# Optimization experiments

Measured on AMD Instinct MI355X. Metric: run time of the kernel, lower is better.

The kernel has to match this reference:

```python
import jax, jax.numpy as jnp
import numpy as np

def setup_inputs() -> dict:
    key = jax.random.key(0)
    k1, k2, k3, k4 = jax.random.split(key, 4)
    B, T, C, D = 4, 4096, 1024, 128
    x = jax.random.normal(k1, (B, T, C), dtype=jnp.float32)
    Wq = jax.random.normal(k2, (C, D), dtype=jnp.float32) * (C ** -0.5)
    Wk = jax.random.normal(k3, (C, D), dtype=jnp.float32) * (C ** -0.5)
    Wv = jax.random.normal(k4, (C, D), dtype=jnp.float32) * (C ** -0.5)
    return {"x": x, "Wq": Wq, "Wk": Wk, "Wv": Wv}

def reference(x, Wq, Wk, Wv):
    # x: [B,T,C]; Wq/Wk/Wv: [C,D] (nn.Linear bias=False => x @ W)
    B, T, C = x.shape
    q = jnp.einsum('btc,cd->btd', x, Wq)  # [B,T,D]
    k = jnp.einsum('btc,cd->btd', x, Wk)
    v = jnp.einsum('btc,cd->btd', x, Wv)
    dk = q.shape[-1]
    scale = dk ** -0.5
    w = jnp.einsum('btd,bsd->bts', q, k) * scale  # [B,T,T]
    causal = jnp.tril(jnp.ones((T, T), dtype=bool))
    w = jnp.where(causal, w, -jnp.inf)
    w = jax.nn.softmax(w, axis=-1)
    # dropout p=0.0 => identity
    attention = jnp.einsum('bts,bsd->btd', w, v)  # [B,T,D]
    return attention
```

## Files before the change

### kernel.cpp

```cpp
#include <hip/hip_runtime.h>
#include <stdint.h>

typedef __bf16 bf16_t;
typedef bf16_t bf16x8 __attribute__((ext_vector_type(8)));
typedef float f32x4 __attribute__((ext_vector_type(4)));
typedef unsigned short us8 __attribute__((ext_vector_type(8)));
typedef unsigned short us4 __attribute__((ext_vector_type(4)));
typedef unsigned int u32x4 __attribute__((ext_vector_type(4)));

#define B_ 4
#define T_ 4096
#define C_ 1024
#define D_ 128

#define NCHUNK_PB 144
#define QSCALE 0.12751744f
#define M0 14.0f

__device__ __forceinline__ uint16_t f2bf(float f) {
    union { float f; uint32_t u; } v; v.f = f;
    uint32_t u = v.u;
    uint32_t r = (u + 0x7fffu + ((u >> 16) & 1u)) >> 16;
    return (uint16_t)r;
}

__device__ __forceinline__ uint16_t bfru(float f) {
    return (uint16_t)((__float_as_uint(f) + 0x8000u) >> 16);
}

__device__ __forceinline__ float bf2f(uint16_t u) {
    return __uint_as_float((uint32_t)u << 16);
}

__device__ __forceinline__ void gload_lds16(const void* g, void* l) {
    __builtin_amdgcn_global_load_lds(
        (const __attribute__((address_space(1))) void*)g,
        (__attribute__((address_space(3))) void*)l, 16, 0, 0);
}

__global__ __launch_bounds__(256) void prep_w(const float* __restrict__ Wq,
                                              const float* __restrict__ Wk,
                                              const float* __restrict__ Wv,
                                              uint16_t* __restrict__ WT) {
    int idx = blockIdx.x * 256 + threadIdx.x;
    if (idx >= 3 * D_ * C_) return;
    int w   = idx / (D_ * C_);
    int rem = idx - w * (D_ * C_);
    int n   = rem / C_;
    int k   = rem - n * C_;
    const float* W = (w == 0) ? Wq : (w == 1) ? Wk : Wv;
    WT[idx] = f2bf(W[(size_t)k * D_ + n]);
}

#define GST 72

__global__ __launch_bounds__(256) void qkv_gemm(const float* __restrict__ x,
                                                const uint16_t* __restrict__ WT,
                                                uint16_t* __restrict__ qb,
                                                uint16_t* __restrict__ kb,
                                                uint16_t* __restrict__ vT) {
    __shared__ __align__(16) uint16_t A_lds[64 * GST];
    __shared__ __align__(16) uint16_t W_lds[128 * GST];

    int tid  = threadIdx.x;
    int lane = tid & 63;
    int wave = tid >> 6;
    int quad = lane >> 4;
    int lx   = lane & 15;
    int wm   = wave >> 1, wn = wave & 1;

    int bx   = blockIdx.x;
    int wsel = bx % 3;
    int m0   = (bx / 3) * 64;
    const uint16_t* Wp = WT + (size_t)wsel * (D_ * C_);

    f32x4 acc[2][4];
    for (int mf = 0; mf < 2; mf++)
        for (int nf = 0; nf < 4; nf++)
            acc[mf][nf] = (f32x4){0.f, 0.f, 0.f, 0.f};

    int arow = tid >> 2, acb = (tid & 3) * 16;
    int wrow = tid >> 1, wcb = (tid & 1) * 32;

    for (int k0 = 0; k0 < C_; k0 += 64) {
        {
            const float* xp = x + (size_t)(m0 + arow) * C_ + k0 + acb;
            uint32_t d[8];
#pragma unroll
            for (int j = 0; j < 4; j++) {
                float4 f = *(const float4*)(xp + j * 4);
                uint32_t u0 = __float_as_uint(f.x) + 0x8000u;
                uint32_t u1 = __float_as_uint(f.y) + 0x8000u;
                uint32_t u2 = __float_as_uint(f.z) + 0x8000u;
                uint32_t u3 = __float_as_uint(f.w) + 0x8000u;
                d[2 * j]     = __builtin_amdgcn_perm(u1, u0, 0x07060302);
                d[2 * j + 1] = __builtin_amdgcn_perm(u3, u2, 0x07060302);
            }
            *(u32x4*)&A_lds[arow * GST + acb]     = (u32x4){d[0], d[1], d[2], d[3]};
            *(u32x4*)&A_lds[arow * GST + acb + 8] = (u32x4){d[4], d[5], d[6], d[7]};
        }
        {
            const uint16_t* wp = Wp + (size_t)wrow * C_ + k0 + wcb;
#pragma unroll
            for (int i = 0; i < 4; i++)
                *(us8*)&W_lds[wrow * GST + wcb + i * 8] = *(const us8*)(wp + i * 8);
        }
        __syncthreads();

#pragma unroll
        for (int kc = 0; kc < 2; kc++) {
            bf16x8 af[2];
#pragma unroll
            for (int mf = 0; mf < 2; mf++)
                af[mf] = *(const bf16x8*)&A_lds[(wm * 32 + mf * 16 + lx) * GST + kc * 32 + quad * 8];
#pragma unroll
            for (int nf = 0; nf < 4; nf++) {
                bf16x8 bf = *(const bf16x8*)&W_lds[(wn * 64 + nf * 16 + lx) * GST + kc * 32 + quad * 8];
                acc[0][nf] = __builtin_amdgcn_mfma_f32_16x16x32_bf16(af[0], bf, acc[0][nf], 0, 0, 0);
                acc[1][nf] = __builtin_amdgcn_mfma_f32_16x16x32_bf16(af[1], bf, acc[1][nf], 0, 0, 0);
            }
        }
        __syncthreads();
    }

    int mrow0 = m0 + wm * 32 + quad * 4;
    if (wsel == 2) {
#pragma unroll
        for (int mf = 0; mf < 2; mf++) {
            int mbase = mrow0 + mf * 16;
            int batch = mbase >> 12;
            int t     = mbase & 4095;
#pragma unroll
            for (int nf = 0; nf < 4; nf++) {
                int n = wn * 64 + nf * 16 + lx;
                us4 pv;
#pragma unroll
                for (int r = 0; r < 4; r++) pv[r] = bfru(acc[mf][nf][r]);
                *(us4*)&vT[(size_t)batch * D_ * T_ + (size_t)n * T_ + t] = pv;
            }
        }
    } else {
        uint16_t* dst = (wsel == 0) ? qb : kb;
        float sc = (wsel == 0) ? QSCALE : 1.0f;
#pragma unroll
        for (int mf = 0; mf < 2; mf++)
#pragma unroll
            for (int nf = 0; nf < 4; nf++) {
                int n = wn * 64 + nf * 16 + lx;
#pragma unroll
                for (int r = 0; r < 4; r++)
                    dst[(size_t)(mrow0 + mf * 16 + r) * D_ + n] = bfru(acc[mf][nf][r] * sc);
            }
    }
}

__global__ __launch_bounds__(256, 2) void attn(const uint16_t* __restrict__ qb,
                                               const uint16_t* __restrict__ kb,
                                               const uint16_t* __restrict__ vT,
                                               uint16_t* __restrict__ part,
                                               float* __restrict__ ml) {
    __shared__ __align__(16) uint16_t K_lds[2][64 * 128];
    __shared__ __align__(16) uint16_t V_lds[2][128 * 64];
    __shared__ __align__(16) uint16_t P_lds[4 * 32 * 64];

    int tid  = threadIdx.x;
    int lane = tid & 63;
    int wave = tid >> 6;
    int quad = lane >> 4;
    int lx   = lane & 15;
    int lx7  = lx & 7;

    int batch = blockIdx.x & 3;
    int L     = NCHUNK_PB - 1 - (blockIdx.x >> 2);
    int a = 0;
    while (a < 7 && 2 * (a + 1) * (a + 2) <= L) a++;
    int rem   = L - 2 * a * (a + 1);
    int jt    = 4 * a + rem / (a + 1);
    int chunk = rem - (rem / (a + 1)) * (a + 1);
    int lidx  = batch * NCHUNK_PB + L;

    int q0     = jt * 128;
    int st0    = chunk * 8;
    int ntiles = min(8, 2 * jt + 2 - st0);

    auto issue_kv = [&](int bi, int tile) {
        int s0i = tile * 64;
        const uint16_t* kB = kb + (size_t)(batch * T_ + s0i) * D_;
#pragma unroll
        for (int j = 0; j < 4; j++) {
            int row = wave * 16 + j * 4 + (lane >> 4);
            int gch = (lane & 15) ^ (row & 7);
            gload_lds16(kB + (size_t)row * D_ + gch * 8,
                        &K_lds[bi][(wave * 16 + j * 4) * 128]);
        }
        const uint16_t* vB = vT + (size_t)batch * D_ * T_ + s0i;
#pragma unroll
        for (int j = 0; j < 4; j++) {
            int row = wave * 32 + j * 8 + (lane >> 3);
            int gch = (lane & 7) ^ (row & 7);
            gload_lds16(vB + (size_t)row * T_ + gch * 8,
                        &V_lds[bi][(wave * 32 + j * 8) * 64]);
        }
    };

    bf16x8 qf[2][4];
#pragma unroll
    for (int mf = 0; mf < 2; mf++) {
        const uint16_t* qp = qb + (size_t)(batch * T_ + q0 + wave * 32 + mf * 16 + lx) * D_ + quad * 8;
#pragma unroll
        for (int kc = 0; kc < 4; kc++) qf[mf][kc] = *(const bf16x8*)(qp + kc * 32);
    }

    f32x4 o[2][8];
#pragma unroll
    for (int mf = 0; mf < 2; mf++)
#pragma unroll
        for (int i = 0; i < 8; i++) o[mf][i] = (f32x4){0.f, 0.f, 0.f, 0.f};
    float l_i[2][4] = {{0.f, 0.f, 0.f, 0.f}, {0.f, 0.f, 0.f, 0.f}};

    issue_kv(0, st0);
    int cur = 0;

    for (int it = 0; it < ntiles; it++) {
        int s0 = (st0 + it) * 64;
        __syncthreads();
        if (it + 1 < ntiles) issue_kv(cur ^ 1, st0 + it + 1);

        f32x4 s[2][4];
#pragma unroll
        for (int mf = 0; mf < 2; mf++)
#pragma unroll
            for (int nf = 0; nf < 4; nf++) s[mf][nf] = (f32x4){0.f, 0.f, 0.f, 0.f};
        __builtin_amdgcn_s_setprio(1);
#pragma unroll
        for (int kc = 0; kc < 4; kc++)
#pragma unroll
            for (int nf = 0; nf < 4; nf++) {
                bf16x8 kf = *(const bf16x8*)&K_lds[cur][(nf * 16 + lx) * 128 + (((kc * 4 + quad) ^ lx7) * 8)];
                s[0][nf] = __builtin_amdgcn_mfma_f32_16x16x32_bf16(qf[0][kc], kf, s[0][nf], 0, 0, 0);
                s[1][nf] = __builtin_amdgcn_mfma_f32_16x16x32_bf16(qf[1][kc], kf, s[1][nf], 0, 0, 0);
            }
        __builtin_amdgcn_s_setprio(0);

        float p[2][4][4];
#pragma unroll
        for (int mf = 0; mf < 2; mf++)
#pragma unroll
            for (int nf = 0; nf < 4; nf++)
#pragma unroll
                for (int r = 0; r < 4; r++) p[mf][nf][r] = s[mf][nf][r];

        if (st0 + it >= 2 * jt) {
#pragma unroll
            for (int mf = 0; mf < 2; mf++) {
                int rowg = q0 + wave * 32 + mf * 16 + quad * 4;
#pragma unroll
                for (int nf = 0; nf < 4; nf++) {
                    int colg = s0 + nf * 16 + lx;
#pragma unroll
                    for (int r = 0; r < 4; r++)
                        if (colg > rowg + r) p[mf][nf][r] = -INFINITY;
                }
            }
        }

#pragma unroll
        for (int mf = 0; mf < 2; mf++) {
#pragma unroll
            for (int nf = 0; nf < 4; nf++)
#pragma unroll
                for (int r = 0; r < 4; r++)
                    p[mf][nf][r] = exp2f(p[mf][nf][r] - M0);
#pragma unroll
            for (int r = 0; r < 4; r++)
                l_i[mf][r] += (p[mf][0][r] + p[mf][1][r]) + (p[mf][2][r] + p[mf][3][r]);
        }

#pragma unroll
        for (int mf = 0; mf < 2; mf++)
#pragma unroll
            for (int nf = 0; nf < 4; nf++)
#pragma unroll
                for (int r = 0; r < 4; r++) {
                    uint32_t u  = __float_as_uint(p[mf][nf][r]) + 0x8000u;
                    uint32_t pu = (uint32_t)__shfl_xor((int)u, 1, 64);
                    uint32_t pk = __builtin_amdgcn_perm(pu, u, 0x07060302);
                    if ((lane & 1) == 0) {
                        int prow = mf * 16 + quad * 4 + r;
                        int pchk = nf * 2 + (lx >> 3);
                        *(uint32_t*)&P_lds[wave * 2048 + prow * 64 + ((pchk ^ (prow & 7)) * 8) + lx7] = pk;
                    }
                }

        bf16x8 pf[2][2];
#pragma unroll
        for (int mf = 0; mf < 2; mf++) {
            pf[mf][0] = *(const bf16x8*)&P_lds[wave * 2048 + (mf * 16 + lx) * 64 + ((quad ^ lx7) * 8)];
            pf[mf][1] = *(const bf16x8*)&P_lds[wave * 2048 + (mf * 16 + lx) * 64 + (((4 + quad) ^ lx7) * 8)];
        }
        __builtin_amdgcn_s_setprio(1);
#pragma unroll
        for (int nf = 0; nf < 8; nf++)
#pragma unroll
            for (int kc = 0; kc < 2; kc++) {
                bf16x8 vf = *(const bf16x8*)&V_lds[cur][(nf * 16 + lx) * 64 + (((kc * 4 + quad) ^ lx7) * 8)];
                o[0][nf] = __builtin_amdgcn_mfma_f32_16x16x32_bf16(pf[0][kc], vf, o[0][nf], 0, 0, 0);
                o[1][nf] = __builtin_amdgcn_mfma_f32_16x16x32_bf16(pf[1][kc], vf, o[1][nf], 0, 0, 0);
            }
        __builtin_amdgcn_s_setprio(0);
        cur ^= 1;
    }

#pragma unroll
    for (int off = 1; off < 16; off <<= 1)
#pragma unroll
        for (int mf = 0; mf < 2; mf++)
#pragma unroll
            for (int r = 0; r < 4; r++)
                l_i[mf][r] += __shfl_xor(l_i[mf][r], off, 64);

    uint16_t* pp = part + (size_t)lidx * (128 * 128);
#pragma unroll
    for (int mf = 0; mf < 2; mf++)
#pragma unroll
        for (int nf = 0; nf < 8; nf++)
#pragma unroll
            for (int r = 0; r < 4; r++) {
                int lrow = wave * 32 + mf * 16 + quad * 4 + r;
                pp[lrow * 128 + nf * 16 + lx] = bfru(o[mf][nf][r]);
            }
    if (lx == 0) {
#pragma unroll
        for (int mf = 0; mf < 2; mf++)
#pragma unroll
            for (int r = 0; r < 4; r++)
                ml[(size_t)lidx * 128 + wave * 32 + mf * 16 + quad * 4 + r] = l_i[mf][r];
    }
}

__global__ __launch_bounds__(256) void combine(const uint16_t* __restrict__ part,
                                               const float* __restrict__ ml,
                                               float* __restrict__ out) {
    int bidx  = blockIdx.x;
    int half  = bidx & 1;
    int jt    = (bidx >> 1) & 31;
    int batch = bidx >> 6;
    int a     = jt >> 2;
    int base  = batch * NCHUNK_PB + 2 * a * (a + 1) + (jt - 4 * a) * (a + 1);
    int nch   = a + 1;

    int tid  = threadIdx.x;
    int lrow = tid >> 1;
    int c0   = half * 64 + (tid & 1) * 32;

    float Lsum = 0.f;
    f32x4 acc[8];
#pragma unroll
    for (int i = 0; i < 8; i++) acc[i] = (f32x4){0.f, 0.f, 0.f, 0.f};

    for (int c = 0; c < nch; c++) {
        Lsum += ml[(size_t)(base + c) * 128 + lrow];
        const uint16_t* p = part + (size_t)(base + c) * (128 * 128) + lrow * 128 + c0;
#pragma unroll
        for (int i = 0; i < 4; i++) {
            us8 v = *(const us8*)(p + i * 8);
#pragma unroll
            for (int j = 0; j < 8; j++)
                acc[i * 2 + (j >> 2)][j & 3] += bf2f(v[j]);
        }
    }
    float inv = 1.f / Lsum;
    size_t row = (size_t)(batch * T_ + jt * 128 + lrow);
#pragma unroll
    for (int i = 0; i < 8; i++)
        *(f32x4*)(out + row * 128 + c0 + i * 4) = acc[i] * inv;
}

extern "C" void kernel_launch(void* const* d_in, const int* in_sizes, int n_in,
                              void* d_out, int out_size, void* d_ws, size_t ws_size,
                              hipStream_t stream) {
    const float* x  = (const float*)d_in[0];
    const float* Wq = (const float*)d_in[1];
    const float* Wk = (const float*)d_in[2];
    const float* Wv = (const float*)d_in[3];
    float* out = (float*)d_out;

    uint16_t* ws = (uint16_t*)d_ws;
    uint16_t* qb = ws;
    uint16_t* kb = qb + (size_t)16384 * 128;
    uint16_t* vT = kb + (size_t)16384 * 128;
    uint16_t* WT = vT + (size_t)16384 * 128;
    uint16_t* part = WT + (size_t)3 * D_ * C_;
    float* ml = (float*)(part + (size_t)4 * NCHUNK_PB * 128 * 128);

    prep_w<<<dim3((3 * D_ * C_ + 255) / 256), dim3(256), 0, stream>>>(Wq, Wk, Wv, WT);
    qkv_gemm<<<dim3(3 * (16384 / 64)), dim3(256), 0, stream>>>(x, WT, qb, kb, vT);
    attn<<<dim3(B_ * NCHUNK_PB), dim3(256), 0, stream>>>(qb, kb, vT, part, ml);
    combine<<<dim3(B_ * 32 * 2), dim3(256), 0, stream>>>(part, ml, out);
}
```

Baseline: 205.5 us.

## Switch attention to 32x32x16 MFMA with register-resident P via permlane32 swap

The attention inner loop now uses 32x32x16 bf16 MFMAs and computes S transposed (K as the A operand), so each lane holds one query row's scores. P is packed with v_cvt_pk_bf16_f32 and rearranged across lane halves with v_permlane32_swap, which removes the per-wave P LDS round trip, its shuffles and its stores. Row sums reduce with a single shuffle instead of a four-step butterfly. The cost is larger accumulator tiles (raising register pressure with two blocks per CU), a different K/V LDS read pattern, and output stores that are less contiguous.

```diff
diff --git a/kernel.cpp b/kernel.cpp
--- a/kernel.cpp
+++ b/kernel.cpp
@@ -4,6 +4,7 @@
 typedef __bf16 bf16_t;
 typedef bf16_t bf16x8 __attribute__((ext_vector_type(8)));
 typedef float f32x4 __attribute__((ext_vector_type(4)));
+typedef float f32x16 __attribute__((ext_vector_type(16)));
 typedef unsigned short us8 __attribute__((ext_vector_type(8)));
 typedef unsigned short us4 __attribute__((ext_vector_type(4)));
 typedef unsigned int u32x4 __attribute__((ext_vector_type(4)));
@@ -30,6 +31,16 @@
 
 __device__ __forceinline__ float bf2f(uint16_t u) {
     return __uint_as_float((uint32_t)u << 16);
+}
+
+__device__ __forceinline__ uint32_t cvtpk(float a, float b) {
+    uint32_t r;
+    asm("v_cvt_pk_bf16_f32 %0, %1, %2" : "=v"(r) : "v"(a), "v"(b));
+    return r;
+}
+
+__device__ __forceinline__ void pl32swap(uint32_t& a, uint32_t& b) {
+    asm("v_permlane32_swap_b32 %0, %1" : "+v"(a), "+v"(b));
 }
 
 __device__ __forceinline__ void gload_lds16(const void* g, void* l) {
@@ -161,14 +172,12 @@
                                                float* __restrict__ ml) {
     __shared__ __align__(16) uint16_t K_lds[2][64 * 128];
     __shared__ __align__(16) uint16_t V_lds[2][128 * 64];
-    __shared__ __align__(16) uint16_t P_lds[4 * 32 * 64];
 
     int tid  = threadIdx.x;
     int lane = tid & 63;
     int wave = tid >> 6;
-    int quad = lane >> 4;
-    int lx   = lane & 15;
-    int lx7  = lx & 7;
+    int q31  = lane & 31;
+    int hi   = lane >> 5;
 
     int batch = blockIdx.x & 3;
     int L     = NCHUNK_PB - 1 - (blockIdx.x >> 2);
@@ -203,20 +212,19 @@
         }
     };
 
-    bf16x8 qf[2][4];
-#pragma unroll
-    for (int mf = 0; mf < 2; mf++) {
-        const uint16_t* qp = qb + (size_t)(batch * T_ + q0 + wave * 32 + mf * 16 + lx) * D_ + quad * 8;
-#pragma unroll
-        for (int kc = 0; kc < 4; kc++) qf[mf][kc] = *(const bf16x8*)(qp + kc * 32);
-    }
-
-    f32x4 o[2][8];
-#pragma unroll
-    for (int mf = 0; mf < 2; mf++)
-#pragma unroll
-        for (int i = 0; i < 8; i++) o[mf][i] = (f32x4){0.f, 0.f, 0.f, 0.f};
-    float l_i[2][4] = {{0.f, 0.f, 0.f, 0.f}, {0.f, 0.f, 0.f, 0.f}};
+    bf16x8 qf[8];
+    {
+        const uint16_t* qp = qb + (size_t)(batch * T_ + q0 + wave * 32 + q31) * D_ + hi * 8;
+#pragma unroll
+        for (int kc = 0; kc < 8; kc++) qf[kc] = *(const bf16x8*)(qp + kc * 16);
+    }
+
+    f32x16 o[4];
+#pragma unroll
+    for (int i = 0; i < 4; i++)
+#pragma unroll
+        for (int r = 0; r < 16; r++) o[i][r] = 0.f;
+    float lsum = 0.f;
 
     issue_kv(0, st0);
     int cur = 0;
@@ -226,116 +234,87 @@
         __syncthreads();
         if (it + 1 < ntiles) issue_kv(cur ^ 1, st0 + it + 1);
 
-        f32x4 s[2][4];
-#pragma unroll
-        for (int mf = 0; mf < 2; mf++)
-#pragma unroll
-            for (int nf = 0; nf < 4; nf++) s[mf][nf] = (f32x4){0.f, 0.f, 0.f, 0.f};
+        f32x16 st[2];
+#pragma unroll
+        for (int nt = 0; nt < 2; nt++)
+#pragma unroll
+            for (int r = 0; r < 16; r++) st[nt][r] = 0.f;
         __builtin_amdgcn_s_setprio(1);
 #pragma unroll
-        for (int kc = 0; kc < 4; kc++)
-#pragma unroll
-            for (int nf = 0; nf < 4; nf++) {
-                bf16x8 kf = *(const bf16x8*)&K_lds[cur][(nf * 16 + lx) * 128 + (((kc * 4 + quad) ^ lx7) * 8)];
-                s[0][nf] = __builtin_amdgcn_mfma_f32_16x16x32_bf16(qf[0][kc], kf, s[0][nf], 0, 0, 0);
-                s[1][nf] = __builtin_amdgcn_mfma_f32_16x16x32_bf16(qf[1][kc], kf, s[1][nf], 0, 0, 0);
+        for (int kc = 0; kc < 8; kc++)
+#pragma unroll
+            for (int nt = 0; nt < 2; nt++) {
+                int row = nt * 32 + q31;
+                bf16x8 kf = *(const bf16x8*)&K_lds[cur][row * 128 + (((kc * 2 + hi) ^ (row & 7)) * 8)];
+                st[nt] = __builtin_amdgcn_mfma_f32_32x32x16_bf16(kf, qf[kc], st[nt], 0, 0, 0);
             }
         __builtin_amdgcn_s_setprio(0);
 
-        float p[2][4][4];
-#pragma unroll
-        for (int mf = 0; mf < 2; mf++)
-#pragma unroll
-            for (int nf = 0; nf < 4; nf++)
-#pragma unroll
-                for (int r = 0; r < 4; r++) p[mf][nf][r] = s[mf][nf][r];
-
         if (st0 + it >= 2 * jt) {
-#pragma unroll
-            for (int mf = 0; mf < 2; mf++) {
-                int rowg = q0 + wave * 32 + mf * 16 + quad * 4;
-#pragma unroll
-                for (int nf = 0; nf < 4; nf++) {
-                    int colg = s0 + nf * 16 + lx;
-#pragma unroll
-                    for (int r = 0; r < 4; r++)
-                        if (colg > rowg + r) p[mf][nf][r] = -INFINITY;
+            int qg = q0 + wave * 32 + q31;
+#pragma unroll
+            for (int nt = 0; nt < 2; nt++)
+#pragma unroll
+                for (int r = 0; r < 16; r++) {
+                    int sg = s0 + nt * 32 + (r & 3) + 8 * (r >> 2) + 4 * hi;
+                    if (sg > qg) st[nt][r] = -INFINITY;
                 }
-            }
-        }
-
-#pragma unroll
-        for (int mf = 0; mf < 2; mf++) {
-#pragma unroll
-            for (int nf = 0; nf < 4; nf++)
-#pragma unroll
-                for (int r = 0; r < 4; r++)
-                    p[mf][nf][r] = exp2f(p[mf][nf][r] - M0);
-#pragma unroll
-            for (int r = 0; r < 4; r++)
-                l_i[mf][r] += (p[mf][0][r] + p[mf][1][r]) + (p[mf][2][r] + p[mf][3][r]);
-        }
-
-#pragma unroll
-        for (int mf = 0; mf < 2; mf++)
-#pragma unroll
-            for (int nf = 0; nf < 4; nf++)
-#pragma unroll
-                for (int r = 0; r < 4; r++) {
-                    uint32_t u  = __float_as_uint(p[mf][nf][r]) + 0x8000u;
-                    uint32_t pu = (uint32_t)__shfl_xor((int)u, 1, 64);
-                    uint32_t pk = __builtin_amdgcn_perm(pu, u, 0x07060302);
-                    if ((lane & 1) == 0) {
-                        int prow = mf * 16 + quad * 4 + r;
-                        int pchk = nf * 2 + (lx >> 3);
-                        *(uint32_t*)&P_lds[wave * 2048 + prow * 64 + ((pchk ^ (prow & 7)) * 8) + lx7] = pk;
-                    }
-                }
-
-        bf16x8 pf[2][2];
-#pragma unroll
-        for (int mf = 0; mf < 2; mf++) {
-            pf[mf][0] = *(const bf16x8*)&P_lds[wave * 2048 + (mf * 16 + lx) * 64 + ((quad ^ lx7) * 8)];
-            pf[mf][1] = *(const bf16x8*)&P_lds[wave * 2048 + (mf * 16 + lx) * 64 + (((4 + quad) ^ lx7) * 8)];
-        }
+        }
+
+#pragma unroll
+        for (int nt = 0; nt < 2; nt++)
+#pragma unroll
+            for (int r = 0; r < 16; r++) {
+                st[nt][r] = exp2f(st[nt][r] - M0);
+                lsum += st[nt][r];
+            }
+
+        bf16x8 pa[4];
+#pragma unroll
+        for (int nt = 0; nt < 2; nt++) {
+            uint32_t x0 = cvtpk(st[nt][0],  st[nt][1]);
+            uint32_t x1 = cvtpk(st[nt][2],  st[nt][3]);
+            uint32_t y0 = cvtpk(st[nt][4],  st[nt][5]);
+            uint32_t y1 = cvtpk(st[nt][6],  st[nt][7]);
+            pl32swap(x0, y0);
+            pl32swap(x1, y1);
+            u32x4 w0 = (u32x4){x0, x1, y0, y1};
+            pa[2 * nt] = *(bf16x8*)&w0;
+            uint32_t z0 = cvtpk(st[nt][8],  st[nt][9]);
+            uint32_t z1 = cvtpk(st[nt][10], st[nt][11]);
+            uint32_t t0 = cvtpk(st[nt][12], st[nt][13]);
+            uint32_t t1 = cvtpk(st[nt][14], st[nt][15]);
+            pl32swap(z0, t0);
+            pl32swap(z1, t1);
+            u32x4 w1 = (u32x4){z0, z1, t0, t1};
+            pa[2 * nt + 1] = *(bf16x8*)&w1;
+        }
+
         __builtin_amdgcn_s_setprio(1);
 #pragma unroll
-        for (int nf = 0; nf < 8; nf++)
-#pragma unroll
-            for (int kc = 0; kc < 2; kc++) {
-                bf16x8 vf = *(const bf16x8*)&V_lds[cur][(nf * 16 + lx) * 64 + (((kc * 4 + quad) ^ lx7) * 8)];
-                o[0][nf] = __builtin_amdgcn_mfma_f32_16x16x32_bf16(pf[0][kc], vf, o[0][nf], 0, 0, 0);
-                o[1][nf] = __builtin_amdgcn_mfma_f32_16x16x32_bf16(pf[1][kc], vf, o[1][nf], 0, 0, 0);
+        for (int sb = 0; sb < 4; sb++)
+#pragma unroll
+            for (int ntd = 0; ntd < 4; ntd++) {
+                int row = ntd * 32 + q31;
+                bf16x8 vf = *(const bf16x8*)&V_lds[cur][row * 64 + (((sb * 2 + hi) ^ (row & 7)) * 8)];
+                o[ntd] = __builtin_amdgcn_mfma_f32_32x32x16_bf16(pa[sb], vf, o[ntd], 0, 0, 0);
             }
         __builtin_amdgcn_s_setprio(0);
         cur ^= 1;
     }
 
-#pragma unroll
-    for (int off = 1; off < 16; off <<= 1)
-#pragma unroll
-        for (int mf = 0; mf < 2; mf++)
-#pragma unroll
-            for (int r = 0; r < 4; r++)
-                l_i[mf][r] += __shfl_xor(l_i[mf][r], off, 64);
+    lsum += __shfl_xor(lsum, 32, 64);
 
     uint16_t* pp = part + (size_t)lidx * (128 * 128);
 #pragma unroll
-    for (int mf = 0; mf < 2; mf++)
-#pragma unroll
-        for (int nf = 0; nf < 8; nf++)
-#pragma unroll
-            for (int r = 0; r < 4; r++) {
-                int lrow = wave * 32 + mf * 16 + quad * 4 + r;
-                pp[lrow * 128 + nf * 16 + lx] = bfru(o[mf][nf][r]);
-            }
-    if (lx == 0) {
-#pragma unroll
-        for (int mf = 0; mf < 2; mf++)
-#pragma unroll
-            for (int r = 0; r < 4; r++)
-                ml[(size_t)lidx * 128 + wave * 32 + mf * 16 + quad * 4 + r] = l_i[mf][r];
-    }
+    for (int ntd = 0; ntd < 4; ntd++)
+#pragma unroll
+        for (int r = 0; r < 16; r++) {
+            int lrow = wave * 32 + (r & 3) + 8 * (r >> 2) + 4 * hi;
+            pp[lrow * 128 + ntd * 32 + q31] = bfru(o[ntd][r]);
+        }
+    if (lane < 32)
+        ml[(size_t)lidx * 128 + wave * 32 + q31] = lsum;
 }
 
 __global__ __launch_bounds__(256) void combine(const uint16_t* __restrict__ part,
```

Measured after the change: 185.6 us. -9.7%, faster.
